# Kernel tuning notes

Measured on AMD Instinct MI355X. Metric: run time of the kernel, lower is better.

## Reference

```python
import jax, jax.numpy as jnp
import numpy as np

# ShapeNet class -> contiguous part-id ranges (from idx2pids in the source)
_STARTS = [0, 4, 6, 8, 12, 16, 19, 22, 24, 28, 30, 36, 38, 41, 44, 47, 50]
_PART_MASK = np.zeros((16, 50), dtype=bool)
for _c in range(16):
    _PART_MASK[_c, _STARTS[_c]:_STARTS[_c + 1]] = True


def setup_inputs() -> dict:
    key = jax.random.key(0)
    k1, k2, k3 = jax.random.split(key, 3)
    B, C, N = 64, 50, 65536
    logits = jax.random.normal(k1, (B, C, N), dtype=jnp.float32)
    targets = jax.random.randint(k2, (B, N), 0, C, dtype=jnp.int64)
    class_labels = jax.random.randint(k3, (B,), 0, 16, dtype=jnp.int64)
    return {"logits": logits, "targets": targets, "class_labels": class_labels}


def reference(logits, targets, class_labels):
    B, C, N = logits.shape
    part_mask = jnp.asarray(_PART_MASK)[class_labels]            # [B, 50] bool
    # mask logits to only the parts valid for each sample's class, then argmax
    masked = jnp.where(part_mask[:, :, None], logits, -jnp.inf)
    pred = jnp.argmax(masked, axis=1)                             # [B, N] int

    # per-(sample, part) counts via segment_sum (fused bincount, no B*N*50 one-hot)
    base = (jnp.arange(B, dtype=jnp.int32) * C)[:, None]          # [B, 1]
    seg_pred = (base + pred.astype(jnp.int32)).reshape(-1)
    seg_tgt = (base + targets.astype(jnp.int32)).reshape(-1)
    ones = jnp.ones(B * N, dtype=jnp.float32)
    match = (pred == targets).reshape(-1).astype(jnp.float32)

    inter = jax.ops.segment_sum(match, seg_pred, num_segments=B * C).reshape(B, C)
    pred_cnt = jax.ops.segment_sum(ones, seg_pred, num_segments=B * C).reshape(B, C)
    gt_cnt = jax.ops.segment_sum(ones, seg_tgt, num_segments=B * C).reshape(B, C)
    union = pred_cnt + gt_cnt - inter                             # [B, 50]

    iou_p = jnp.where(union == 0, 1.0, inter / jnp.maximum(union, 1.0))
    pmf = part_mask.astype(jnp.float32)
    batch_iou = (iou_p * pmf).sum(axis=1) / pmf.sum(axis=1)       # [B]
    return batch_iou.mean(), pred
```

## Files before the change

kernel.cpp:

```cpp
#include <hip/hip_runtime.h>

#define BB 64
#define CC 50
#define NN 65536

__constant__ int c_starts[17] = {0, 4, 6, 8, 12, 16, 19, 22, 24, 28, 30, 36, 38, 41, 44, 47, 50};

__global__ __launch_bounds__(256) void miou_main(
    const float* __restrict__ logits,
    const int*   __restrict__ targets,
    const int*   __restrict__ cls,
    float*       __restrict__ out,
    int*         __restrict__ cnt)
{
    __shared__ int s_cnt[3 * CC];
    const int b     = (int)blockIdx.x >> 6;
    const int chunk = (int)blockIdx.x & 63;

    for (int i = threadIdx.x; i < 3 * CC; i += 256) s_cnt[i] = 0;
    __syncthreads();

    const int cl = cls[b];
    const int s0 = c_starts[cl];
    const int s1 = c_starts[cl + 1];

    const int n0 = (chunk << 10) + ((int)threadIdx.x << 2);
    const float* lg = logits + (size_t)b * (size_t)CC * NN;

    const int4 tgt = *(const int4*)(targets + (size_t)b * NN + n0);

    float4 best = *(const float4*)(lg + (size_t)s0 * NN + n0);
    int bx = s0, by = s0, bz = s0, bw = s0;
    for (int c = s0 + 1; c < s1; ++c) {
        float4 v = *(const float4*)(lg + (size_t)c * NN + n0);
        if (v.x > best.x) { best.x = v.x; bx = c; }
        if (v.y > best.y) { best.y = v.y; by = c; }
        if (v.z > best.z) { best.z = v.z; bz = c; }
        if (v.w > best.w) { best.w = v.w; bw = c; }
    }

    float* po = out + 1 + (size_t)b * NN + n0;
    po[0] = (float)bx; po[1] = (float)by; po[2] = (float)bz; po[3] = (float)bw;

    atomicAdd(&s_cnt[CC + bx], 1);
    atomicAdd(&s_cnt[CC + by], 1);
    atomicAdd(&s_cnt[CC + bz], 1);
    atomicAdd(&s_cnt[CC + bw], 1);
    atomicAdd(&s_cnt[2 * CC + tgt.x], 1);
    atomicAdd(&s_cnt[2 * CC + tgt.y], 1);
    atomicAdd(&s_cnt[2 * CC + tgt.z], 1);
    atomicAdd(&s_cnt[2 * CC + tgt.w], 1);
    if (bx == tgt.x) atomicAdd(&s_cnt[bx], 1);
    if (by == tgt.y) atomicAdd(&s_cnt[by], 1);
    if (bz == tgt.z) atomicAdd(&s_cnt[bz], 1);
    if (bw == tgt.w) atomicAdd(&s_cnt[bw], 1);

    __syncthreads();
    for (int i = threadIdx.x; i < 3 * CC; i += 256) {
        int v = s_cnt[i];
        if (v) atomicAdd(&cnt[(i / CC) * (BB * CC) + b * CC + (i % CC)], v);
    }
}

__global__ __launch_bounds__(64) void miou_final(
    const int* __restrict__ cls,
    const int* __restrict__ cnt,
    float*     __restrict__ out)
{
    const int b  = threadIdx.x;
    const int cl = cls[b];
    const int s0 = c_starts[cl], s1 = c_starts[cl + 1];
    float sum = 0.f;
    for (int c = s0; c < s1; ++c) {
        float inter = (float)cnt[b * CC + c];
        float pc    = (float)cnt[BB * CC + b * CC + c];
        float gc    = (float)cnt[2 * BB * CC + b * CC + c];
        float un    = pc + gc - inter;
        float iou   = (un == 0.f) ? 1.f : inter / fmaxf(un, 1.f);
        sum += iou;
    }
    float biou = sum / (float)(s1 - s0);
    for (int off = 32; off; off >>= 1) biou += __shfl_down(biou, off);
    if (b == 0) out[0] = biou / (float)BB;
}

extern "C" void kernel_launch(void* const* d_in, const int* in_sizes, int n_in,
                              void* d_out, int out_size, void* d_ws, size_t ws_size,
                              hipStream_t stream) {
    const float* logits  = (const float*)d_in[0];
    const int*   targets = (const int*)d_in[1];
    const int*   cls     = (const int*)d_in[2];
    float*       out     = (float*)d_out;
    int*         cnt     = (int*)d_ws;

    hipMemsetAsync(cnt, 0, 3 * BB * CC * sizeof(int), stream);

    miou_main<<<dim3(BB * 64), dim3(256), 0, stream>>>(logits, targets, cls, out, cnt);
    miou_final<<<1, 64, 0, stream>>>(cls, cnt, out);
}
```

Baseline: 902.1 us.

## Process 16 points per thread, pack counters into one LDS atomic, nontemporal stores

```diff
diff --git a/kernel.cpp b/kernel.cpp
--- a/kernel.cpp
+++ b/kernel.cpp
@@ -3,62 +3,82 @@
 #define BB 64
 #define CC 50
 #define NN 65536
+#define TPB 256
+#define PTS 16
+#define CHUNK (TPB * PTS)
+#define NCHUNK (NN / CHUNK)
 
 __constant__ int c_starts[17] = {0, 4, 6, 8, 12, 16, 19, 22, 24, 28, 30, 36, 38, 41, 44, 47, 50};
 
-__global__ __launch_bounds__(256) void miou_main(
+__global__ __launch_bounds__(TPB) void miou_main(
     const float* __restrict__ logits,
     const int*   __restrict__ targets,
     const int*   __restrict__ cls,
     float*       __restrict__ out,
     int*         __restrict__ cnt)
 {
-    __shared__ int s_cnt[3 * CC];
-    const int b     = (int)blockIdx.x >> 6;
-    const int chunk = (int)blockIdx.x & 63;
+    __shared__ int s_pi[CC];
+    __shared__ int s_gt[CC];
 
-    for (int i = threadIdx.x; i < 3 * CC; i += 256) s_cnt[i] = 0;
+    const int b     = (int)blockIdx.x / NCHUNK;
+    const int chunk = (int)blockIdx.x % NCHUNK;
+
+    for (int i = threadIdx.x; i < CC; i += TPB) { s_pi[i] = 0; s_gt[i] = 0; }
     __syncthreads();
 
     const int cl = cls[b];
-    const int s0 = c_starts[cl];
-    const int s1 = c_starts[cl + 1];
+    const int s0 = c_starts[cl], s1 = c_starts[cl + 1];
+    const int n0 = chunk * CHUNK + (int)threadIdx.x * PTS;
 
-    const int n0 = (chunk << 10) + ((int)threadIdx.x << 2);
-    const float* lg = logits + (size_t)b * (size_t)CC * NN;
+    const float* lg = logits + (size_t)b * CC * NN + n0;
 
-    const int4 tgt = *(const int4*)(targets + (size_t)b * NN + n0);
-
-    float4 best = *(const float4*)(lg + (size_t)s0 * NN + n0);
-    int bx = s0, by = s0, bz = s0, bw = s0;
+    float4 best[4];
+    int4   idx[4];
+    {
+        const float4* p = (const float4*)(lg + (size_t)s0 * NN);
+        #pragma unroll
+        for (int q = 0; q < 4; ++q) { best[q] = p[q]; idx[q] = make_int4(s0, s0, s0, s0); }
+    }
     for (int c = s0 + 1; c < s1; ++c) {
-        float4 v = *(const float4*)(lg + (size_t)c * NN + n0);
-        if (v.x > best.x) { best.x = v.x; bx = c; }
-        if (v.y > best.y) { best.y = v.y; by = c; }
-        if (v.z > best.z) { best.z = v.z; bz = c; }
-        if (v.w > best.w) { best.w = v.w; bw = c; }
+        const float4* p = (const float4*)(lg + (size_t)c * NN);
+        #pragma unroll
+        for (int q = 0; q < 4; ++q) {
+            float4 v = p[q];
+            if (v.x > best[q].x) { best[q].x = v.x; idx[q].x = c; }
+            if (v.y > best[q].y) { best[q].y = v.y; idx[q].y = c; }
+            if (v.z > best[q].z) { best[q].z = v.z; idx[q].z = c; }
+            if (v.w > best[q].w) { best[q].w = v.w; idx[q].w = c; }
+        }
     }
 
-    float* po = out + 1 + (size_t)b * NN + n0;
-    po[0] = (float)bx; po[1] = (float)by; po[2] = (float)bz; po[3] = (float)bw;
+    const int4* tg = (const int4*)(targets + (size_t)b * NN + n0);
+    float*      po = out + 1 + (size_t)b * NN + n0;
 
-    atomicAdd(&s_cnt[CC + bx], 1);
-    atomicAdd(&s_cnt[CC + by], 1);
-    atomicAdd(&s_cnt[CC + bz], 1);
-    atomicAdd(&s_cnt[CC + bw], 1);
-    atomicAdd(&s_cnt[2 * CC + tgt.x], 1);
-    atomicAdd(&s_cnt[2 * CC + tgt.y], 1);
-    atomicAdd(&s_cnt[2 * CC + tgt.z], 1);
-    atomicAdd(&s_cnt[2 * CC + tgt.w], 1);
-    if (bx == tgt.x) atomicAdd(&s_cnt[bx], 1);
-    if (by == tgt.y) atomicAdd(&s_cnt[by], 1);
-    if (bz == tgt.z) atomicAdd(&s_cnt[bz], 1);
-    if (bw == tgt.w) atomicAdd(&s_cnt[bw], 1);
+    #pragma unroll
+    for (int q = 0; q < 4; ++q) {
+        int4 t = tg[q];
+        __builtin_nontemporal_store((float)idx[q].x, po + q * 4 + 0);
+        __builtin_nontemporal_store((float)idx[q].y, po + q * 4 + 1);
+        __builtin_nontemporal_store((float)idx[q].z, po + q * 4 + 2);
+        __builtin_nontemporal_store((float)idx[q].w, po + q * 4 + 3);
+        atomicAdd(&s_pi[idx[q].x], 1 + ((int)(idx[q].x == t.x) << 16));
+        atomicAdd(&s_pi[idx[q].y], 1 + ((int)(idx[q].y == t.y) << 16));
+        atomicAdd(&s_pi[idx[q].z], 1 + ((int)(idx[q].z == t.z) << 16));
+        atomicAdd(&s_pi[idx[q].w], 1 + ((int)(idx[q].w == t.w) << 16));
+        atomicAdd(&s_gt[t.x], 1);
+        atomicAdd(&s_gt[t.y], 1);
+        atomicAdd(&s_gt[t.z], 1);
+        atomicAdd(&s_gt[t.w], 1);
+    }
 
     __syncthreads();
-    for (int i = threadIdx.x; i < 3 * CC; i += 256) {
-        int v = s_cnt[i];
-        if (v) atomicAdd(&cnt[(i / CC) * (BB * CC) + b * CC + (i % CC)], v);
+    for (int i = threadIdx.x; i < CC; i += TPB) {
+        int pi = s_pi[i], g = s_gt[i];
+        if (pi) {
+            atomicAdd(&cnt[b * CC + i],           pi >> 16);
+            atomicAdd(&cnt[BB * CC + b * CC + i], pi & 0xffff);
+        }
+        if (g) atomicAdd(&cnt[2 * BB * CC + b * CC + i], g);
     }
 }
 
@@ -95,6 +115,6 @@
 
     hipMemsetAsync(cnt, 0, 3 * BB * CC * sizeof(int), stream);
 
-    miou_main<<<dim3(BB * 64), dim3(256), 0, stream>>>(logits, targets, cls, out, cnt);
+    miou_main<<<dim3(BB * NCHUNK), dim3(TPB), 0, stream>>>(logits, targets, cls, out, cnt);
     miou_final<<<1, 64, 0, stream>>>(cls, cnt, out);
 }
```

Result: no change. 919.4 us (+1.9%).
